# Optimization experiments

Hardware: AMD Instinct MI355X
Metric: run time of the kernel (lower is better)

## Reference

```python
import jax, jax.numpy as jnp
import numpy as np

B, S, N, F_IN = 4, 256, 500, 32
D, L = 64, 2
TEMP = 0.5
EPS = 1e-5

def gelu(x):
    return jax.nn.gelu(x, approximate=False)  # torch default GELU (erf)

def layernorm(h, g, b):
    mu = h.mean(-1, keepdims=True)
    var = ((h - mu) ** 2).mean(-1, keepdims=True)
    return (h - mu) * jax.lax.rsqrt(var + EPS) * g + b

def gru_last(x_seq, Wih, Whh, bih, bhh):
    # x_seq: [B, T, I]; torch nn.GRU gate math, h0 = 0; returns final hidden [B, D]
    xp = jnp.einsum('bti,gi->btg', x_seq, Wih) + bih  # precompute input gates [B, T, 3D]
    d = Whh.shape[1]
    def step(h, xpt):
        gh = h @ Whh.T + bhh
        xr, xz, xn = jnp.split(xpt, 3, axis=-1)
        hr, hz, hn = jnp.split(gh, 3, axis=-1)
        r = jax.nn.sigmoid(xr + hr)
        z = jax.nn.sigmoid(xz + hz)
        n = jnp.tanh(xn + r * hn)
        return (1.0 - z) * n + z * h, None
    h0 = jnp.zeros((x_seq.shape[0], d), x_seq.dtype)
    h, _ = jax.lax.scan(step, h0, xp.transpose(1, 0, 2))
    return h

def forward(x, ip_W, ip_b, from_embed, to_embed, gl_W, gl_b, gl_g, gl_be,
            Wih_s, Whh_s, bih_s, bhh_s, Wih_m, Whh_m, bih_m, bhh_m,
            Wih_l, Whh_l, bih_l, bhh_l, dh_W1, dh_b1, dh_W2, dh_b2):
    # input_proj: Linear + GELU (Dropout is identity in eval)
    x = gelu(jnp.einsum('bsnf,df->bsnd', x, ip_W) + ip_b)  # [B,S,N,D]
    # learned adjacency: softmax over destination nodes
    adj = jax.nn.softmax((from_embed @ to_embed.T) / TEMP, axis=-1)  # [N,N]
    for i in range(gl_W.shape[0]):
        agg = jnp.einsum('bsnd,nm->bsmd', x, adj)
        h = gelu(jnp.einsum('bsnd,ed->bsne', x + agg, gl_W[i]) + gl_b[i])
        x = layernorm(h, gl_g[i], gl_be[i])
    b, s, n, d = x.shape
    x_flat = x.reshape(b, s, n * d)
    h_s = gru_last(x_flat[:, -10:, :], Wih_s, Whh_s, bih_s, bhh_s)
    h_m = gru_last(x_flat[:, -20:, :], Wih_m, Whh_m, bih_m, bhh_m)
    h_l = gru_last(x_flat, Wih_l, Whh_l, bih_l, bhh_l)
    h = jnp.concatenate([h_s, h_m, h_l], axis=-1)  # [B, 3D]
    h = gelu(h @ dh_W1.T + dh_b1)
    return h @ dh_W2.T + dh_b2  # direction logits [B, N]

def setup_inputs():
    key = jax.random.key(0)
    it = iter(jax.random.split(key, 40))
    rn = lambda shape, s=0.02: jax.random.normal(next(it), shape, jnp.float32) * s
    I = N * D
    return {
        'x': jax.random.normal(next(it), (B, S, N, F_IN), jnp.float32),
        'ip_W': rn((D, F_IN)), 'ip_b': jnp.zeros((D,), jnp.float32),
        'from_embed': rn((N, 32), 0.1), 'to_embed': rn((N, 32), 0.1),
        'gl_W': rn((L, D, D)), 'gl_b': jnp.zeros((L, D), jnp.float32),
        'gl_g': jnp.ones((L, D), jnp.float32), 'gl_be': jnp.zeros((L, D), jnp.float32),
        'Wih_s': rn((3 * D, I)), 'Whh_s': rn((3 * D, D)),
        'bih_s': jnp.zeros((3 * D,), jnp.float32), 'bhh_s': jnp.zeros((3 * D,), jnp.float32),
        'Wih_m': rn((3 * D, I)), 'Whh_m': rn((3 * D, D)),
        'bih_m': jnp.zeros((3 * D,), jnp.float32), 'bhh_m': jnp.zeros((3 * D,), jnp.float32),
        'Wih_l': rn((3 * D, I)), 'Whh_l': rn((3 * D, D)),
        'bih_l': jnp.zeros((3 * D,), jnp.float32), 'bhh_l': jnp.zeros((3 * D,), jnp.float32),
        'dh_W1': rn((D, 3 * D)), 'dh_b1': jnp.zeros((D,), jnp.float32),
        'dh_W2': rn((N, D)), 'dh_b2': jnp.zeros((N,), jnp.float32),
    }

def reference(x, ip_W, ip_b, from_embed, to_embed, gl_W, gl_b, gl_g, gl_be,
              Wih_s, Whh_s, bih_s, bhh_s, Wih_m, Whh_m, bih_m, bhh_m,
              Wih_l, Whh_l, bih_l, bhh_l, dh_W1, dh_b1, dh_W2, dh_b2):
    return forward(x, ip_W, ip_b, from_embed, to_embed, gl_W, gl_b, gl_g, gl_be,
                   Wih_s, Whh_s, bih_s, bhh_s, Wih_m, Whh_m, bih_m, bhh_m,
                   Wih_l, Whh_l, bih_l, bhh_l, dh_W1, dh_b1, dh_W2, dh_b2)
```

## Files before the change

kernel.cpp:

```cpp
#include <hip/hip_runtime.h>
#include <math.h>

#define NN 500
#define DD 64
#define NPAD 512
#define COLS 65536
#define BS_TOT 1024
#define I_DIM 32000
#define KS_GRU 40
#define KSL 800

typedef __attribute__((ext_vector_type(8))) short bf16x8;
typedef __attribute__((ext_vector_type(4))) float f32x4;

__device__ __forceinline__ float gelu_f(float x) {
    return 0.5f * x * (1.0f + erff(x * 0.70710678118654752440f));
}

__device__ __forceinline__ unsigned short bf16_rn(float x) {
    unsigned int u = __float_as_uint(x);
    unsigned int r = u + 0x7FFFu + ((u >> 16) & 1u);
    return (unsigned short)(r >> 16);
}
__device__ __forceinline__ float bf16_tof(unsigned short h) {
    return __uint_as_float(((unsigned int)h) << 16);
}
__device__ __forceinline__ unsigned int pack_hl(float x) {
    unsigned short h = bf16_rn(x);
    unsigned short l = bf16_rn(x - bf16_tof(h));
    return (unsigned int)h | ((unsigned int)l << 16);
}
__device__ __forceinline__ float unpack_val(unsigned int u) {
    return __uint_as_float(u << 16) + __uint_as_float(u & 0xFFFF0000u);
}
__device__ __forceinline__ void split4(float4 v, short4& h4, short4& l4) {
    h4.x = (short)bf16_rn(v.x); l4.x = (short)bf16_rn(v.x - bf16_tof((unsigned short)h4.x));
    h4.y = (short)bf16_rn(v.y); l4.y = (short)bf16_rn(v.y - bf16_tof((unsigned short)h4.y));
    h4.z = (short)bf16_rn(v.z); l4.z = (short)bf16_rn(v.z - bf16_tof((unsigned short)h4.z));
    h4.w = (short)bf16_rn(v.w); l4.w = (short)bf16_rn(v.w - bf16_tof((unsigned short)h4.w));
}

__device__ __forceinline__ int swz_k(int row, int kbyte) {
    return kbyte ^ (((row >> 3) & 3) << 4);
}

__global__ __launch_bounds__(512)
void adj_kernel(const float* __restrict__ fe, const float* __restrict__ te,
                short* __restrict__ adjTh, short* __restrict__ adjTl)
{
    __shared__ float fr[32];
    __shared__ float red[8];
    __shared__ float red2[8];
    const int n = blockIdx.x;
    const int tid = threadIdx.x;
    if (tid < 32) fr[tid] = fe[n * 32 + tid];
    __syncthreads();
    const int m = tid;
    float s = -1e30f;
    if (m < NN) {
        float acc = 0.f;
        #pragma unroll
        for (int f = 0; f < 32; ++f) acc += fr[f] * te[m * 32 + f];
        s = acc * 2.0f;
    }
    float v = s;
    #pragma unroll
    for (int off = 32; off; off >>= 1) v = fmaxf(v, __shfl_xor(v, off));
    if ((tid & 63) == 0) red[tid >> 6] = v;
    __syncthreads();
    float bmax = red[0];
    #pragma unroll
    for (int i = 1; i < 8; ++i) bmax = fmaxf(bmax, red[i]);
    float e = (m < NN) ? expf(s - bmax) : 0.f;
    float v2 = e;
    #pragma unroll
    for (int off = 32; off; off >>= 1) v2 += __shfl_xor(v2, off);
    if ((tid & 63) == 0) red2[tid >> 6] = v2;
    __syncthreads();
    float bsum = 0.f;
    #pragma unroll
    for (int i = 0; i < 8; ++i) bsum += red2[i];
    if (m < NN) {
        float p = e / bsum;
        unsigned short h = bf16_rn(p);
        adjTh[(size_t)m * NPAD + n] = (short)h;
        adjTl[(size_t)m * NPAD + n] = (short)bf16_rn(p - bf16_tof(h));
    }
}

__global__ __launch_bounds__(256)
void wsplit_kernel(const float* __restrict__ W, short* __restrict__ H,
                   short* __restrict__ L, int n4)
{
    int i = blockIdx.x * 256 + threadIdx.x;
    if (i < n4) {
        float4 v = *(const float4*)&W[i * 4];
        short4 h4, l4;
        split4(v, h4, l4);
        *(short4*)&H[i * 4] = h4;
        *(short4*)&L[i * 4] = l4;
    }
}

__global__ __launch_bounds__(256)
void proj_mfma_kernel(const float* __restrict__ xin,
                      const short* __restrict__ Wh, const short* __restrict__ Wl,
                      const float* __restrict__ ipb, unsigned int* __restrict__ Xhl)
{
    const int tid  = threadIdx.x;
    const int lane = tid & 63;
    const int wave = tid >> 6;
    const int q = lane >> 4, r16 = lane & 15;
    const size_t row0 = (size_t)blockIdx.x * 128 + wave * 32;

    float bB[4];
    #pragma unroll
    for (int ci = 0; ci < 4; ++ci) bB[ci] = ipb[ci * 16 + r16];

    bf16x8 wh[4], wl[4];
    #pragma unroll
    for (int ci = 0; ci < 4; ++ci) {
        int off = (ci * 16 + r16) * 32 + q * 8;
        wh[ci] = *(const bf16x8*)&Wh[off];
        wl[ci] = *(const bf16x8*)&Wl[off];
    }

    f32x4 acc[2][4];
    #pragma unroll
    for (int i = 0; i < 2; ++i)
        #pragma unroll
        for (int j = 0; j < 4; ++j) acc[i][j] = (f32x4){0.f, 0.f, 0.f, 0.f};

    #pragma unroll
    for (int mi = 0; mi < 2; ++mi) {
        const size_t row = row0 + mi * 16 + r16;
        const int n = (int)(row >> 10), bs = (int)(row & 1023);
        const float* src = &xin[((size_t)bs * NN + n) * 32 + q * 8];
        float4 v0 = *(const float4*)src;
        float4 v1 = *(const float4*)(src + 4);
        short4 h0, l0, h1, l1;
        split4(v0, h0, l0);
        split4(v1, h1, l1);
        bf16x8 ah, al;
        ah[0] = h0.x; ah[1] = h0.y; ah[2] = h0.z; ah[3] = h0.w;
        ah[4] = h1.x; ah[5] = h1.y; ah[6] = h1.z; ah[7] = h1.w;
        al[0] = l0.x; al[1] = l0.y; al[2] = l0.z; al[3] = l0.w;
        al[4] = l1.x; al[5] = l1.y; al[6] = l1.z; al[7] = l1.w;
        #pragma unroll
        for (int ci = 0; ci < 4; ++ci) {
            acc[mi][ci] = __builtin_amdgcn_mfma_f32_16x16x32_bf16(ah, wh[ci], acc[mi][ci], 0, 0, 0);
            acc[mi][ci] = __builtin_amdgcn_mfma_f32_16x16x32_bf16(ah, wl[ci], acc[mi][ci], 0, 0, 0);
            acc[mi][ci] = __builtin_amdgcn_mfma_f32_16x16x32_bf16(al, wh[ci], acc[mi][ci], 0, 0, 0);
        }
    }

    #pragma unroll
    for (int mi = 0; mi < 2; ++mi) {
        #pragma unroll
        for (int rg = 0; rg < 4; ++rg) {
            size_t grow = row0 + mi * 16 + q * 4 + rg;
            #pragma unroll
            for (int ci = 0; ci < 4; ++ci) {
                float y = gelu_f(acc[mi][ci][rg] + bB[ci]);
                Xhl[grow * 64 + ci * 16 + r16] = pack_hl(y);
            }
        }
    }
}

__global__ __launch_bounds__(256)
void agg_mfma_kernel(const unsigned int* __restrict__ Xhl,
                     const short* __restrict__ adjTh, const short* __restrict__ adjTl,
                     unsigned int* __restrict__ Yhl)
{
    __shared__ __align__(16) short Ah[128 * 40];
    __shared__ __align__(16) short Al[128 * 40];
    __shared__ __align__(16) short Bh[128 * 40];
    __shared__ __align__(16) short Bl[128 * 40];

    const int tid  = threadIdx.x;
    const int lane = tid & 63;
    const int wave = tid >> 6;
    const int wm = (wave >> 1) * 64;
    const int wc = (wave & 1) * 64;
    const int q = lane >> 4, r16 = lane & 15;
    const int c0 = blockIdx.x * 128;
    const int m0 = blockIdx.y * 128;

    const int sa_m = tid >> 1, sa_kh = tid & 1;
    const int sb_c = tid & 127, sb_kh = tid >> 7;

    f32x4 acc[4][4];
    #pragma unroll
    for (int i = 0; i < 4; ++i)
        #pragma unroll
        for (int j = 0; j < 4; ++j) acc[i][j] = (f32x4){0.f, 0.f, 0.f, 0.f};

    for (int kc = 0; kc < 16; ++kc) {
        const int k0 = kc * 32;
        {
            const size_t base = (size_t)(m0 + sa_m) * NPAD + k0 + sa_kh * 16;
            bf16x8 h0 = *(const bf16x8*)&adjTh[base];
            bf16x8 h1 = *(const bf16x8*)&adjTh[base + 8];
            bf16x8 l0 = *(const bf16x8*)&adjTl[base];
            bf16x8 l1 = *(const bf16x8*)&adjTl[base + 8];
            char* rowH = (char*)Ah + sa_m * 80;
            char* rowL = (char*)Al + sa_m * 80;
            *(bf16x8*)(rowH + swz_k(sa_m, sa_kh * 32))      = h0;
            *(bf16x8*)(rowH + swz_k(sa_m, sa_kh * 32 + 16)) = h1;
            *(bf16x8*)(rowL + swz_k(sa_m, sa_kh * 32))      = l0;
            *(bf16x8*)(rowL + swz_k(sa_m, sa_kh * 32 + 16)) = l1;
        }
        {
            const size_t cb = (size_t)(c0 + sb_c);
            unsigned int u[16];
            #pragma unroll
            for (int j = 0; j < 16; ++j) {
                int kk = k0 + sb_kh * 16 + j;
                u[j] = (kk < NN) ? Xhl[(size_t)kk * COLS + cb] : 0u;
            }
            bf16x8 h0, h1, l0, l1;
            #pragma unroll
            for (int j = 0; j < 8; ++j) {
                h0[j] = (short)(u[j] & 0xFFFFu);     l0[j] = (short)(u[j] >> 16);
                h1[j] = (short)(u[8 + j] & 0xFFFFu); l1[j] = (short)(u[8 + j] >> 16);
            }
            char* rowH = (char*)Bh + sb_c * 80;
            char* rowL = (char*)Bl + sb_c * 80;
            int kb0 = swz_k(sb_c, sb_kh * 32);
            int kb1 = swz_k(sb_c, sb_kh * 32 + 16);
            *(bf16x8*)(rowH + kb0) = h0; *(bf16x8*)(rowH + kb1) = h1;
            *(bf16x8*)(rowL + kb0) = l0; *(bf16x8*)(rowL + kb1) = l1;
        }
        __syncthreads();
        bf16x8 ah[4], al[4];
        #pragma unroll
        for (int mi = 0; mi < 4; ++mi) {
            int row = wm + mi * 16 + r16;
            int kb = swz_k(row, q * 16);
            ah[mi] = *(const bf16x8*)((const char*)Ah + row * 80 + kb);
            al[mi] = *(const bf16x8*)((const char*)Al + row * 80 + kb);
        }
        #pragma unroll
        for (int ci = 0; ci < 4; ++ci) {
            int row = wc + ci * 16 + r16;
            int kb = swz_k(row, q * 16);
            bf16x8 bh = *(const bf16x8*)((const char*)Bh + row * 80 + kb);
            bf16x8 bl = *(const bf16x8*)((const char*)Bl + row * 80 + kb);
            #pragma unroll
            for (int mi = 0; mi < 4; ++mi) {
                acc[mi][ci] = __builtin_amdgcn_mfma_f32_16x16x32_bf16(ah[mi], bh, acc[mi][ci], 0, 0, 0);
                acc[mi][ci] = __builtin_amdgcn_mfma_f32_16x16x32_bf16(ah[mi], bl, acc[mi][ci], 0, 0, 0);
                acc[mi][ci] = __builtin_amdgcn_mfma_f32_16x16x32_bf16(al[mi], bh, acc[mi][ci], 0, 0, 0);
            }
        }
        __syncthreads();
    }
    #pragma unroll
    for (int mi = 0; mi < 4; ++mi) {
        #pragma unroll
        for (int r = 0; r < 4; ++r) {
            int m = m0 + wm + mi * 16 + q * 4 + r;
            if (m < NN) {
                #pragma unroll
                for (int ci = 0; ci < 4; ++ci) {
                    size_t idx = (size_t)m * COLS + c0 + wc + ci * 16 + r16;
                    float y = acc[mi][ci][r] + unpack_val(Xhl[idx]);
                    Yhl[idx] = pack_hl(y);
                }
            }
        }
    }
}

__global__ __launch_bounds__(256)
void hln_stream_kernel(unsigned int* __restrict__ Xio,
                       const short* __restrict__ Wh, const short* __restrict__ Wl,
                       const float* __restrict__ glb, const float* __restrict__ glg,
                       const float* __restrict__ glbe)
{
    const int tid  = threadIdx.x;
    const int lane = tid & 63;
    const int wave = tid >> 6;
    const int q = lane >> 4, r16 = lane & 15;
    const size_t row0 = (size_t)blockIdx.x * 128 + wave * 32;

    float bB2[4], bG2[4], bE2[4];
    #pragma unroll
    for (int ci = 0; ci < 4; ++ci) {
        int e = ci * 16 + r16;
        bB2[ci] = glb[e]; bG2[ci] = glg[e]; bE2[ci] = glbe[e];
    }

    f32x4 acc[2][4];
    #pragma unroll
    for (int i = 0; i < 2; ++i)
        #pragma unroll
        for (int j = 0; j < 4; ++j) acc[i][j] = (f32x4){0.f, 0.f, 0.f, 0.f};

    #pragma unroll
    for (int kh = 0; kh < 2; ++kh) {
        bf16x8 wh[4], wl[4];
        #pragma unroll
        for (int ci = 0; ci < 4; ++ci) {
            int off = (ci * 16 + r16) * 64 + kh * 32 + q * 8;
            wh[ci] = *(const bf16x8*)&Wh[off];
            wl[ci] = *(const bf16x8*)&Wl[off];
        }
        #pragma unroll
        for (int mi = 0; mi < 2; ++mi) {
            const size_t row = row0 + mi * 16 + r16;
            const unsigned int* src = &Xio[row * 64 + kh * 32 + q * 8];
            uint4 u0 = *(const uint4*)src;
            uint4 u1 = *(const uint4*)(src + 4);
            bf16x8 ah, al;
            ah[0] = (short)(u0.x & 0xFFFFu); al[0] = (short)(u0.x >> 16);
            ah[1] = (short)(u0.y & 0xFFFFu); al[1] = (short)(u0.y >> 16);
            ah[2] = (short)(u0.z & 0xFFFFu); al[2] = (short)(u0.z >> 16);
            ah[3] = (short)(u0.w & 0xFFFFu); al[3] = (short)(u0.w >> 16);
            ah[4] = (short)(u1.x & 0xFFFFu); al[4] = (short)(u1.x >> 16);
            ah[5] = (short)(u1.y & 0xFFFFu); al[5] = (short)(u1.y >> 16);
            ah[6] = (short)(u1.z & 0xFFFFu); al[6] = (short)(u1.z >> 16);
            ah[7] = (short)(u1.w & 0xFFFFu); al[7] = (short)(u1.w >> 16);
            #pragma unroll
            for (int ci = 0; ci < 4; ++ci) {
                acc[mi][ci] = __builtin_amdgcn_mfma_f32_16x16x32_bf16(ah, wh[ci], acc[mi][ci], 0, 0, 0);
                acc[mi][ci] = __builtin_amdgcn_mfma_f32_16x16x32_bf16(ah, wl[ci], acc[mi][ci], 0, 0, 0);
                acc[mi][ci] = __builtin_amdgcn_mfma_f32_16x16x32_bf16(al, wh[ci], acc[mi][ci], 0, 0, 0);
            }
        }
    }

    #pragma unroll
    for (int mi = 0; mi < 2; ++mi) {
        #pragma unroll
        for (int rg = 0; rg < 4; ++rg) {
            float h[4];
            float s1 = 0.f;
            #pragma unroll
            for (int ci = 0; ci < 4; ++ci) {
                h[ci] = gelu_f(acc[mi][ci][rg] + bB2[ci]);
                s1 += h[ci];
            }
            #pragma unroll
            for (int off = 1; off < 16; off <<= 1) s1 += __shfl_xor(s1, off);
            float mu = s1 * (1.f / 64.f);
            float s2 = 0.f;
            #pragma unroll
            for (int ci = 0; ci < 4; ++ci) { float dc = h[ci] - mu; s2 += dc * dc; }
            #pragma unroll
            for (int off = 1; off < 16; off <<= 1) s2 += __shfl_xor(s2, off);
            float rs = 1.f / sqrtf(s2 * (1.f / 64.f) + 1e-5f);
            size_t grow = row0 + mi * 16 + q * 4 + rg;
            #pragma unroll
            for (int ci = 0; ci < 4; ++ci) {
                float y = (h[ci] - mu) * rs * bG2[ci] + bE2[ci];
                Xio[grow * 64 + ci * 16 + r16] = pack_hl(y);
            }
        }
    }
}

__global__ __launch_bounds__(256)
void wconv_kernel(const float* __restrict__ W0, const float* __restrict__ W1,
                  const float* __restrict__ W2,
                  short* __restrict__ h0, short* __restrict__ l0,
                  short* __restrict__ h1, short* __restrict__ l1,
                  short* __restrict__ h2, short* __restrict__ l2)
{
    const int gi = blockIdx.y;
    const float* W = (gi == 0) ? W0 : (gi == 1) ? W1 : W2;
    short* H = (gi == 0) ? h0 : (gi == 1) ? h1 : h2;
    short* L = (gi == 0) ? l0 : (gi == 1) ? l1 : l2;
    const size_t i = ((size_t)blockIdx.x * 256 + threadIdx.x) * 4;
    float4 v = *(const float4*)&W[i];
    short4 h4, l4;
    split4(v, h4, l4);
    *(short4*)&H[i] = h4;
    *(short4*)&L[i] = l4;
}

__global__ __launch_bounds__(256)
void gru_pre_mfma_kernel(const unsigned int* __restrict__ Xhl,
                         const short* __restrict__ Wh0, const short* __restrict__ Wl0,
                         const short* __restrict__ Wh1, const short* __restrict__ Wl1,
                         const short* __restrict__ Wh2, const short* __restrict__ Wl2,
                         float* __restrict__ p0, float* __restrict__ p1,
                         float* __restrict__ p2)
{
    __shared__ __align__(16) short Ah[64 * 40];
    __shared__ __align__(16) short Al[64 * 40];
    __shared__ __align__(16) short Bh[192 * 40];
    __shared__ __align__(16) short Bl[192 * 40];

    const int bid = blockIdx.x;
    int gi, mtid, ks;
    if (bid < 40)       { gi = 0; mtid = 0;             ks = bid; }
    else if (bid < 120) { int r = bid - 40;  gi = 1; mtid = r & 1;  ks = r >> 1; }
    else                { int r = bid - 120; gi = 2; mtid = r & 15; ks = r >> 4; }
    const short* Wh = (gi == 0) ? Wh0 : (gi == 1) ? Wh1 : Wh2;
    const short* Wl = (gi == 0) ? Wl0 : (gi == 1) ? Wl1 : Wl2;
    float* partial  = (gi == 0) ? p0 : (gi == 1) ? p1 : p2;
    const int Trows = (gi == 0) ? 10 : (gi == 1) ? 20 : 256;
    const int toff  = (gi == 0) ? 246 : (gi == 1) ? 236 : 0;
    const int M     = (gi == 0) ? 40 : (gi == 1) ? 80 : 1024;
    const int R0 = mtid * 64;

    const int tid  = threadIdx.x;
    const int lane = tid & 63;
    const int wave = tid >> 6;
    const int wr = (wave & 1) * 32;
    const int wg = (wave >> 1) * 96;
    const int q = lane >> 4, r16 = lane & 15;

    const int sa_r = tid >> 2, sa_kq = tid & 3;
    const bool vldA = (R0 + sa_r < M);
    int btA = 0;
    if (vldA) { int R = R0 + sa_r; int b = R / Trows, t = R - b * Trows; btA = b * 256 + toff + t; }

    f32x4 acc[2][6];
    #pragma unroll
    for (int i = 0; i < 2; ++i)
        #pragma unroll
        for (int j = 0; j < 6; ++j) acc[i][j] = (f32x4){0.f, 0.f, 0.f, 0.f};

    for (int c = 0; c < KSL / 32; ++c) {
        const int k0 = ks * KSL + c * 32;
        {
            const int kk = k0 + sa_kq * 8;
            const int nn = kk >> 6, d0 = kk & 63;
            uint4 u0 = make_uint4(0u, 0u, 0u, 0u), u1 = u0;
            if (vldA) {
                const unsigned int* src = &Xhl[((size_t)nn * BS_TOT + btA) * 64 + d0];
                u0 = *(const uint4*)src;
                u1 = *(const uint4*)(src + 4);
            }
            short4 h0 = make_short4((short)(u0.x & 0xFFFF), (short)(u0.y & 0xFFFF),
                                    (short)(u0.z & 0xFFFF), (short)(u0.w & 0xFFFF));
            short4 l0 = make_short4((short)(u0.x >> 16), (short)(u0.y >> 16),
                                    (short)(u0.z >> 16), (short)(u0.w >> 16));
            short4 h1 = make_short4((short)(u1.x & 0xFFFF), (short)(u1.y & 0xFFFF),
                                    (short)(u1.z & 0xFFFF), (short)(u1.w & 0xFFFF));
            short4 l1 = make_short4((short)(u1.x >> 16), (short)(u1.y >> 16),
                                    (short)(u1.z >> 16), (short)(u1.w >> 16));
            int kb = swz_k(sa_r, sa_kq * 16);
            char* rowH = (char*)Ah + sa_r * 80;
            char* rowL = (char*)Al + sa_r * 80;
            *(short4*)(rowH + kb) = h0; *(short4*)(rowH + kb + 8) = h1;
            *(short4*)(rowL + kb) = l0; *(short4*)(rowL + kb + 8) = l1;
        }
        #pragma unroll
        for (int l = 0; l < 3; ++l) {
            int idx = tid + l * 256;
            int g = idx >> 2, kq = idx & 3;
            const size_t src = (size_t)g * I_DIM + k0 + kq * 8;
            bf16x8 hv = *(const bf16x8*)&Wh[src];
            bf16x8 lv = *(const bf16x8*)&Wl[src];
            int kb = swz_k(g, kq * 16);
            *(bf16x8*)((char*)Bh + g * 80 + kb) = hv;
            *(bf16x8*)((char*)Bl + g * 80 + kb) = lv;
        }
        __syncthreads();
        bf16x8 ah[2], al[2];
        #pragma unroll
        for (int mi = 0; mi < 2; ++mi) {
            int row = wr + mi * 16 + r16;
            int kb = swz_k(row, q * 16);
            ah[mi] = *(const bf16x8*)((const char*)Ah + row * 80 + kb);
            al[mi] = *(const bf16x8*)((const char*)Al + row * 80 + kb);
        }
        #pragma unroll
        for (int ci = 0; ci < 6; ++ci) {
            int grow = wg + ci * 16 + r16;
            int kb = swz_k(grow, q * 16);
            bf16x8 bh = *(const bf16x8*)((const char*)Bh + grow * 80 + kb);
            bf16x8 bl = *(const bf16x8*)((const char*)Bl + grow * 80 + kb);
            #pragma unroll
            for (int mi = 0; mi < 2; ++mi) {
                acc[mi][ci] = __builtin_amdgcn_mfma_f32_16x16x32_bf16(ah[mi], bh, acc[mi][ci], 0, 0, 0);
                acc[mi][ci] = __builtin_amdgcn_mfma_f32_16x16x32_bf16(ah[mi], bl, acc[mi][ci], 0, 0, 0);
                acc[mi][ci] = __builtin_amdgcn_mfma_f32_16x16x32_bf16(al[mi], bh, acc[mi][ci], 0, 0, 0);
            }
        }
        __syncthreads();
    }
    #pragma unroll
    for (int mi = 0; mi < 2; ++mi) {
        #pragma unroll
        for (int r = 0; r < 4; ++r) {
            int R = R0 + wr + mi * 16 + q * 4 + r;
            if (R < M) {
                #pragma unroll
                for (int ci = 0; ci < 6; ++ci)
                    partial[((size_t)ks * M + R) * 192 + wg + ci * 16 + r16] = acc[mi][ci][r];
            }
        }
    }
}

__global__ __launch_bounds__(192)
void gru_reduce_fused_kernel(const float* __restrict__ p0, const float* __restrict__ p1,
                             const float* __restrict__ p2,
                             const float* __restrict__ bih0, const float* __restrict__ bih1,
                             const float* __restrict__ bih2,
                             float* __restrict__ xp0, float* __restrict__ xp1,
                             float* __restrict__ xp2)
{
    int r = blockIdx.x;
    const float* partial; const float* bih; float* xp; int M;
    if (r < 40)       { partial = p0; bih = bih0; xp = xp0; M = 40; }
    else if (r < 120) { r -= 40;  partial = p1; bih = bih1; xp = xp1; M = 80; }
    else              { r -= 120; partial = p2; bih = bih2; xp = xp2; M = 1024; }
    const int g = threadIdx.x;
    float acc = bih[g];
    for (int ks = 0; ks < KS_GRU; ++ks)
        acc += partial[((size_t)ks * M + r) * 192 + g];
    xp[(size_t)r * 192 + g] = acc;
}

__global__ __launch_bounds__(192)
void gru_scan_kernel(const float* __restrict__ xp_s, const float* __restrict__ xp_m,
                     const float* __restrict__ xp_l,
                     const float* __restrict__ Whh_s, const float* __restrict__ Whh_m,
                     const float* __restrict__ Whh_l,
                     const float* __restrict__ bhh_s, const float* __restrict__ bhh_m,
                     const float* __restrict__ bhh_l,
                     float* __restrict__ hcat)
{
    __shared__ float h[64];
    __shared__ float gh[192];
    const int blk = blockIdx.x;
    const int g3 = blk >> 2, b = blk & 3;
    const float* xp  = (g3 == 0) ? xp_s : (g3 == 1) ? xp_m : xp_l;
    const float* Whh = (g3 == 0) ? Whh_s : (g3 == 1) ? Whh_m : Whh_l;
    const float* bhh = (g3 == 0) ? bhh_s : (g3 == 1) ? bhh_m : bhh_l;
    const int T = (g3 == 0) ? 10 : (g3 == 1) ? 20 : 256;
    const int g = threadIdx.x;

    float w[64];
    #pragma unroll
    for (int k4 = 0; k4 < 16; ++k4) {
        float4 v = *(const float4*)&Whh[g * 64 + k4 * 4];
        w[k4 * 4 + 0] = v.x; w[k4 * 4 + 1] = v.y;
        w[k4 * 4 + 2] = v.z; w[k4 * 4 + 3] = v.w;
    }
    const float bh = bhh[g];
    if (g < 64) h[g] = 0.f;

    const float* xpb = xp + (size_t)b * T * 192;
    float xr_c = 0.f, xz_c = 0.f, xn_c = 0.f;
    if (g < 64) { xr_c = xpb[g]; xz_c = xpb[64 + g]; xn_c = xpb[128 + g]; }
    __syncthreads();

    for (int t = 0; t < T; ++t) {
        float xr_n = 0.f, xz_n = 0.f, xn_n = 0.f;
        if (t + 1 < T && g < 64) {
            const float* xq = xpb + (size_t)(t + 1) * 192;
            xr_n = xq[g]; xz_n = xq[64 + g]; xn_n = xq[128 + g];
        }
        float a0 = 0.f, a1 = 0.f, a2 = 0.f, a3 = 0.f;
        #pragma unroll
        for (int k4 = 0; k4 < 16; ++k4) {
            float4 hv = ((const float4*)h)[k4];
            a0 += hv.x * w[k4 * 4 + 0];
            a1 += hv.y * w[k4 * 4 + 1];
            a2 += hv.z * w[k4 * 4 + 2];
            a3 += hv.w * w[k4 * 4 + 3];
        }
        gh[g] = bh + ((a0 + a1) + (a2 + a3));
        __syncthreads();
        if (g < 64) {
            float hr = gh[g], hz = gh[64 + g], hn = gh[128 + g];
            float r = 1.f / (1.f + __expf(-(xr_c + hr)));
            float z = 1.f / (1.f + __expf(-(xz_c + hz)));
            float pre = xn_c + r * hn;
            float e2 = __expf(2.f * pre);
            float nv = 1.f - 2.f / (e2 + 1.f);
            h[g] = (1.f - z) * nv + z * h[g];
        }
        __syncthreads();
        xr_c = xr_n; xz_c = xz_n; xn_c = xn_n;
    }
    if (g < 64) hcat[b * 192 + g3 * 64 + g] = h[g];
}

__global__ __launch_bounds__(512)
void head_kernel(const float* __restrict__ hcat,
                 const float* __restrict__ W1, const float* __restrict__ b1,
                 const float* __restrict__ W2, const float* __restrict__ b2,
                 float* __restrict__ out)
{
    __shared__ float hc[4][192];
    __shared__ float h1[4][64];
    const int tid = threadIdx.x;
    for (int i = tid; i < 768; i += 512) hc[i / 192][i % 192] = hcat[i];
    __syncthreads();
    if (tid < 256) {
        int b = tid >> 6, e = tid & 63;
        float acc = b1[e];
        #pragma unroll
        for (int k = 0; k < 192; ++k) acc += hc[b][k] * W1[e * 192 + k];
        h1[b][e] = gelu_f(acc);
    }
    __syncthreads();
    for (int o = tid; o < 2000; o += 512) {
        int b = o / 500, n = o % 500;
        float acc = b2[n];
        #pragma unroll
        for (int k = 0; k < 64; ++k) acc += h1[b][k] * W2[n * 64 + k];
        out[o] = acc;
    }
}

extern "C" void kernel_launch(void* const* d_in, const int* in_sizes, int n_in,
                              void* d_out, int out_size, void* d_ws, size_t ws_size,
                              hipStream_t stream)
{
    (void)in_sizes; (void)n_in; (void)out_size; (void)ws_size;
    const float* x    = (const float*)d_in[0];
    const float* ipW  = (const float*)d_in[1];
    const float* ipb  = (const float*)d_in[2];
    const float* fe   = (const float*)d_in[3];
    const float* te   = (const float*)d_in[4];
    const float* glW  = (const float*)d_in[5];
    const float* glb  = (const float*)d_in[6];
    const float* glg  = (const float*)d_in[7];
    const float* glbe = (const float*)d_in[8];
    const float* Wih[3] = {(const float*)d_in[9],  (const float*)d_in[13], (const float*)d_in[17]};
    const float* Whh[3] = {(const float*)d_in[10], (const float*)d_in[14], (const float*)d_in[18]};
    const float* bih[3] = {(const float*)d_in[11], (const float*)d_in[15], (const float*)d_in[19]};
    const float* bhh[3] = {(const float*)d_in[12], (const float*)d_in[16], (const float*)d_in[20]};
    const float* W1 = (const float*)d_in[21];
    const float* b1 = (const float*)d_in[22];
    const float* W2 = (const float*)d_in[23];
    const float* b2 = (const float*)d_in[24];
    float* out = (float*)d_out;

    unsigned int* Xhl = (unsigned int*)d_ws;
    unsigned int* Yhl = Xhl + 32768000;
    short* adjTh = (short*)(Yhl + 32768000);
    short* adjTl = adjTh + NPAD * NPAD;
    short* glWh  = adjTl + NPAD * NPAD;
    short* glWl  = glWh + 8192;
    short* ipWh  = glWl + 8192;
    short* ipWl  = ipWh + 2048;
    short* wbase = (short*)Yhl;
    short* Wh0 = wbase;
    short* Wl0 = Wh0 + 6144000;
    short* Wh1 = Wl0 + 6144000;
    short* Wl1 = Wh1 + 6144000;
    short* Wh2 = Wl1 + 6144000;
    short* Wl2 = Wh2 + 6144000;
    float* pbase = (float*)Yhl + 18432000;
    float* part0 = pbase;
    float* part1 = part0 + 307200;
    float* part2 = part1 + 614400;
    float* xp0   = part2 + 7864320;
    float* xp1   = xp0 + 7680;
    float* xp2   = xp1 + 15360;
    float* hcat  = xp2 + 196608;

    hipMemsetAsync(adjTh, 0, (size_t)NPAD * NPAD * 2 * sizeof(short), stream);
    adj_kernel<<<NN, 512, 0, stream>>>(fe, te, adjTh, adjTl);
    wsplit_kernel<<<8, 256, 0, stream>>>(glW, glWh, glWl, 2048);
    wsplit_kernel<<<2, 256, 0, stream>>>(ipW, ipWh, ipWl, 512);
    proj_mfma_kernel<<<4000, 256, 0, stream>>>(x, ipWh, ipWl, ipb, Xhl);

    agg_mfma_kernel<<<dim3(512, 4), 256, 0, stream>>>(Xhl, adjTh, adjTl, Yhl);
    hln_stream_kernel<<<4000, 256, 0, stream>>>(Yhl, glWh, glWl, glb, glg, glbe);
    agg_mfma_kernel<<<dim3(512, 4), 256, 0, stream>>>(Yhl, adjTh, adjTl, Xhl);
    hln_stream_kernel<<<4000, 256, 0, stream>>>(Xhl, glWh + 4096, glWl + 4096,
                                                glb + 64, glg + 64, glbe + 64);

    wconv_kernel<<<dim3(6000, 3), 256, 0, stream>>>(Wih[0], Wih[1], Wih[2],
                                                    Wh0, Wl0, Wh1, Wl1, Wh2, Wl2);
    gru_pre_mfma_kernel<<<760, 256, 0, stream>>>(Xhl, Wh0, Wl0, Wh1, Wl1, Wh2, Wl2,
                                                 part0, part1, part2);
    gru_reduce_fused_kernel<<<1144, 192, 0, stream>>>(part0, part1, part2,
                                                      bih[0], bih[1], bih[2],
                                                      xp0, xp1, xp2);
    gru_scan_kernel<<<12, 192, 0, stream>>>(xp0, xp1, xp2,
                                            Whh[0], Whh[1], Whh[2],
                                            bhh[0], bhh[1], bhh[2], hcat);
    head_kernel<<<1, 512, 0, stream>>>(hcat, W1, b1, W2, b2, out);
}
```

Measured before the change: 844.8 us.

## Double-buffer shared-memory tiles in aggregation GEMM and remap GRU block order

The adjacency aggregation kernel now keeps two shared-memory buffers. Global loads for the next K chunk are issued before the MFMA work on the current chunk and written to the other buffer afterwards, which removes one barrier per iteration and overlaps memory latency with compute. Shared memory use doubles and register pressure rises because the prefetched values are held across the MFMA loop, which may lower occupancy. The GRU input-projection kernel also changes its block-to-tile mapping so that consecutive blocks walk the K-split for one M tile, which changes the order in which weight and activation data are reused across blocks.

```diff
diff --git a/kernel.cpp b/kernel.cpp
--- a/kernel.cpp
+++ b/kernel.cpp
@@ -173,10 +173,10 @@
                      const short* __restrict__ adjTh, const short* __restrict__ adjTl,
                      unsigned int* __restrict__ Yhl)
 {
-    __shared__ __align__(16) short Ah[128 * 40];
-    __shared__ __align__(16) short Al[128 * 40];
-    __shared__ __align__(16) short Bh[128 * 40];
-    __shared__ __align__(16) short Bl[128 * 40];
+    __shared__ __align__(16) short Ah[2][128 * 40];
+    __shared__ __align__(16) short Al[2][128 * 40];
+    __shared__ __align__(16) short Bh[2][128 * 40];
+    __shared__ __align__(16) short Bl[2][128 * 40];
 
     const int tid  = threadIdx.x;
     const int lane = tid & 63;
@@ -189,6 +189,7 @@
 
     const int sa_m = tid >> 1, sa_kh = tid & 1;
     const int sb_c = tid & 127, sb_kh = tid >> 7;
+    const size_t cb = (size_t)(c0 + sb_c);
 
     f32x4 acc[4][4];
     #pragma unroll
@@ -196,57 +197,71 @@
         #pragma unroll
         for (int j = 0; j < 4; ++j) acc[i][j] = (f32x4){0.f, 0.f, 0.f, 0.f};
 
+    {
+        const size_t base = (size_t)(m0 + sa_m) * NPAD + sa_kh * 16;
+        bf16x8 h0 = *(const bf16x8*)&adjTh[base];
+        bf16x8 h1 = *(const bf16x8*)&adjTh[base + 8];
+        bf16x8 l0 = *(const bf16x8*)&adjTl[base];
+        bf16x8 l1 = *(const bf16x8*)&adjTl[base + 8];
+        char* rowH = (char*)Ah[0] + sa_m * 80;
+        char* rowL = (char*)Al[0] + sa_m * 80;
+        *(bf16x8*)(rowH + swz_k(sa_m, sa_kh * 32))      = h0;
+        *(bf16x8*)(rowH + swz_k(sa_m, sa_kh * 32 + 16)) = h1;
+        *(bf16x8*)(rowL + swz_k(sa_m, sa_kh * 32))      = l0;
+        *(bf16x8*)(rowL + swz_k(sa_m, sa_kh * 32 + 16)) = l1;
+
+        unsigned int u[16];
+        #pragma unroll
+        for (int j = 0; j < 16; ++j) {
+            int kk = sb_kh * 16 + j;
+            u[j] = (kk < NN) ? Xhl[(size_t)kk * COLS + cb] : 0u;
+        }
+        bf16x8 bh0, bh1, bl0, bl1;
+        #pragma unroll
+        for (int j = 0; j < 8; ++j) {
+            bh0[j] = (short)(u[j] & 0xFFFFu);     bl0[j] = (short)(u[j] >> 16);
+            bh1[j] = (short)(u[8 + j] & 0xFFFFu); bl1[j] = (short)(u[8 + j] >> 16);
+        }
+        char* rbH = (char*)Bh[0] + sb_c * 80;
+        char* rbL = (char*)Bl[0] + sb_c * 80;
+        int kb0 = swz_k(sb_c, sb_kh * 32);
+        int kb1 = swz_k(sb_c, sb_kh * 32 + 16);
+        *(bf16x8*)(rbH + kb0) = bh0; *(bf16x8*)(rbH + kb1) = bh1;
+        *(bf16x8*)(rbL + kb0) = bl0; *(bf16x8*)(rbL + kb1) = bl1;
+    }
+    __syncthreads();
+
     for (int kc = 0; kc < 16; ++kc) {
-        const int k0 = kc * 32;
-        {
-            const size_t base = (size_t)(m0 + sa_m) * NPAD + k0 + sa_kh * 16;
-            bf16x8 h0 = *(const bf16x8*)&adjTh[base];
-            bf16x8 h1 = *(const bf16x8*)&adjTh[base + 8];
-            bf16x8 l0 = *(const bf16x8*)&adjTl[base];
-            bf16x8 l1 = *(const bf16x8*)&adjTl[base + 8];
-            char* rowH = (char*)Ah + sa_m * 80;
-            char* rowL = (char*)Al + sa_m * 80;
-            *(bf16x8*)(rowH + swz_k(sa_m, sa_kh * 32))      = h0;
-            *(bf16x8*)(rowH + swz_k(sa_m, sa_kh * 32 + 16)) = h1;
-            *(bf16x8*)(rowL + swz_k(sa_m, sa_kh * 32))      = l0;
-            *(bf16x8*)(rowL + swz_k(sa_m, sa_kh * 32 + 16)) = l1;
-        }
-        {
-            const size_t cb = (size_t)(c0 + sb_c);
-            unsigned int u[16];
+        const int cur = kc & 1;
+        bf16x8 nAh0, nAh1, nAl0, nAl1;
+        unsigned int nu[16];
+        if (kc < 15) {
+            const int k0n = (kc + 1) * 32;
+            const size_t base = (size_t)(m0 + sa_m) * NPAD + k0n + sa_kh * 16;
+            nAh0 = *(const bf16x8*)&adjTh[base];
+            nAh1 = *(const bf16x8*)&adjTh[base + 8];
+            nAl0 = *(const bf16x8*)&adjTl[base];
+            nAl1 = *(const bf16x8*)&adjTl[base + 8];
             #pragma unroll
             for (int j = 0; j < 16; ++j) {
-                int kk = k0 + sb_kh * 16 + j;
-                u[j] = (kk < NN) ? Xhl[(size_t)kk * COLS + cb] : 0u;
-            }
-            bf16x8 h0, h1, l0, l1;
-            #pragma unroll
-            for (int j = 0; j < 8; ++j) {
-                h0[j] = (short)(u[j] & 0xFFFFu);     l0[j] = (short)(u[j] >> 16);
-                h1[j] = (short)(u[8 + j] & 0xFFFFu); l1[j] = (short)(u[8 + j] >> 16);
-            }
-            char* rowH = (char*)Bh + sb_c * 80;
-            char* rowL = (char*)Bl + sb_c * 80;
-            int kb0 = swz_k(sb_c, sb_kh * 32);
-            int kb1 = swz_k(sb_c, sb_kh * 32 + 16);
-            *(bf16x8*)(rowH + kb0) = h0; *(bf16x8*)(rowH + kb1) = h1;
-            *(bf16x8*)(rowL + kb0) = l0; *(bf16x8*)(rowL + kb1) = l1;
-        }
-        __syncthreads();
+                int kk = k0n + sb_kh * 16 + j;
+                nu[j] = (kk < NN) ? Xhl[(size_t)kk * COLS + cb] : 0u;
+            }
+        }
         bf16x8 ah[4], al[4];
         #pragma unroll
         for (int mi = 0; mi < 4; ++mi) {
             int row = wm + mi * 16 + r16;
             int kb = swz_k(row, q * 16);
-            ah[mi] = *(const bf16x8*)((const char*)Ah + row * 80 + kb);
-            al[mi] = *(const bf16x8*)((const char*)Al + row * 80 + kb);
+            ah[mi] = *(const bf16x8*)((const char*)Ah[cur] + row * 80 + kb);
+            al[mi] = *(const bf16x8*)((const char*)Al[cur] + row * 80 + kb);
         }
         #pragma unroll
         for (int ci = 0; ci < 4; ++ci) {
             int row = wc + ci * 16 + r16;
             int kb = swz_k(row, q * 16);
-            bf16x8 bh = *(const bf16x8*)((const char*)Bh + row * 80 + kb);
-            bf16x8 bl = *(const bf16x8*)((const char*)Bl + row * 80 + kb);
+            bf16x8 bh = *(const bf16x8*)((const char*)Bh[cur] + row * 80 + kb);
+            bf16x8 bl = *(const bf16x8*)((const char*)Bl[cur] + row * 80 + kb);
             #pragma unroll
             for (int mi = 0; mi < 4; ++mi) {
                 acc[mi][ci] = __builtin_amdgcn_mfma_f32_16x16x32_bf16(ah[mi], bh, acc[mi][ci], 0, 0, 0);
@@ -254,8 +269,30 @@
                 acc[mi][ci] = __builtin_amdgcn_mfma_f32_16x16x32_bf16(al[mi], bh, acc[mi][ci], 0, 0, 0);
             }
         }
+        if (kc < 15) {
+            const int nb = cur ^ 1;
+            char* rowH = (char*)Ah[nb] + sa_m * 80;
+            char* rowL = (char*)Al[nb] + sa_m * 80;
+            *(bf16x8*)(rowH + swz_k(sa_m, sa_kh * 32))      = nAh0;
+            *(bf16x8*)(rowH + swz_k(sa_m, sa_kh * 32 + 16)) = nAh1;
+            *(bf16x8*)(rowL + swz_k(sa_m, sa_kh * 32))      = nAl0;
+            *(bf16x8*)(rowL + swz_k(sa_m, sa_kh * 32 + 16)) = nAl1;
+            bf16x8 bh0, bh1, bl0, bl1;
+            #pragma unroll
+            for (int j = 0; j < 8; ++j) {
+                bh0[j] = (short)(nu[j] & 0xFFFFu);     bl0[j] = (short)(nu[j] >> 16);
+                bh1[j] = (short)(nu[8 + j] & 0xFFFFu); bl1[j] = (short)(nu[8 + j] >> 16);
+            }
+            char* rbH = (char*)Bh[nb] + sb_c * 80;
+            char* rbL = (char*)Bl[nb] + sb_c * 80;
+            int kb0 = swz_k(sb_c, sb_kh * 32);
+            int kb1 = swz_k(sb_c, sb_kh * 32 + 16);
+            *(bf16x8*)(rbH + kb0) = bh0; *(bf16x8*)(rbH + kb1) = bh1;
+            *(bf16x8*)(rbL + kb0) = bl0; *(bf16x8*)(rbL + kb1) = bl1;
+        }
         __syncthreads();
     }
+
     #pragma unroll
     for (int mi = 0; mi < 4; ++mi) {
         #pragma unroll
@@ -396,8 +433,8 @@
     const int bid = blockIdx.x;
     int gi, mtid, ks;
     if (bid < 40)       { gi = 0; mtid = 0;             ks = bid; }
-    else if (bid < 120) { int r = bid - 40;  gi = 1; mtid = r & 1;  ks = r >> 1; }
-    else                { int r = bid - 120; gi = 2; mtid = r & 15; ks = r >> 4; }
+    else if (bid < 120) { int r = bid - 40;  gi = 1; ks = r % 40; mtid = r / 40; }
+    else                { int r = bid - 120; gi = 2; ks = r % 40; mtid = r / 40; }
     const short* Wh = (gi == 0) ? Wh0 : (gi == 1) ? Wh1 : Wh2;
     const short* Wl = (gi == 0) ? Wl0 : (gi == 1) ? Wl1 : Wl2;
     float* partial  = (gi == 0) ? p0 : (gi == 1) ? p1 : p2;
```

New measurement: 768.7 us. -9.0%, faster.
